# Performance work log

Measured on AMD Instinct MI355X. Metric: run time of the kernel, lower is better.

## Reference

```python
import jax, jax.numpy as jnp
import numpy as np

B, T, C, H = 2, 4096, 512, 8
D = C // H          # head_size = 64
FF = 4 * C          # 2048
EPS = 1e-5


def _layernorm(x, g, b):
    mu = jnp.mean(x, axis=-1, keepdims=True)
    var = jnp.mean(jnp.square(x - mu), axis=-1, keepdims=True)
    return (x - mu) * jax.lax.rsqrt(var + EPS) * g + b


def setup_inputs() -> dict:
    key = jax.random.key(0)
    ks = jax.random.split(key, 10)
    s = 0.02
    return {
        "x":  jax.random.normal(ks[0], (B, T, C), dtype=jnp.float32),
        # per-head K/Q/V linears (bias=False) packed as [C, C] = concat over heads
        "Wq": jax.random.normal(ks[1], (C, C), dtype=jnp.float32) * s,
        "Wk": jax.random.normal(ks[2], (C, C), dtype=jnp.float32) * s,
        "Wv": jax.random.normal(ks[3], (C, C), dtype=jnp.float32) * s,
        "Wo": jax.random.normal(ks[4], (C, C), dtype=jnp.float32) * s,
        "bo": jnp.zeros((C,), dtype=jnp.float32),
        "W1": jax.random.normal(ks[5], (C, FF), dtype=jnp.float32) * s,
        "b1": jnp.zeros((FF,), dtype=jnp.float32),
        "W2": jax.random.normal(ks[6], (FF, C), dtype=jnp.float32) * s,
        "b2": jnp.zeros((C,), dtype=jnp.float32),
        "g1": jnp.ones((C,), dtype=jnp.float32),
        "be1": jnp.zeros((C,), dtype=jnp.float32),
        "g2": jnp.ones((C,), dtype=jnp.float32),
        "be2": jnp.zeros((C,), dtype=jnp.float32),
    }


def reference(x, Wq, Wk, Wv, Wo, bo, W1, b1, W2, b2, g1, be1, g2, be2):
    # --- self-attention on ln1(x), residual add ---
    h = _layernorm(x, g1, be1)                              # [B,T,C]
    q = (h @ Wq).reshape(B, T, H, D)
    k = (h @ Wk).reshape(B, T, H, D)
    v = (h @ Wv).reshape(B, T, H, D)
    # NOTE: original scales by C**-0.5 (n_embd), NOT head_size**-0.5
    scores = jnp.einsum("bthd,bshd->bhts", q, k) * (C ** -0.5)  # [B,H,T,T]
    causal = jnp.tril(jnp.ones((T, T), dtype=bool))
    scores = jnp.where(causal, scores, -jnp.inf)
    wei = jax.nn.softmax(scores, axis=-1)                   # dropout = identity (eval)
    attn = jnp.einsum("bhts,bshd->bthd", wei, v).reshape(B, T, C)
    x = x + (attn @ Wo + bo)                                # proj dropout = identity
    # --- feed-forward on ln2(x), residual add ---
    h2 = _layernorm(x, g2, be2)
    ff = jax.nn.relu(h2 @ W1 + b1) @ W2 + b2                # dropout = identity
    return x + ff
```

## Files before the change

kernel.cpp:

```cpp
#include <hip/hip_runtime.h>

typedef __attribute__((ext_vector_type(8))) __bf16 bf16x8;
typedef __attribute__((ext_vector_type(4))) __bf16 bf16x4;
typedef __attribute__((ext_vector_type(4))) float f32x4;
typedef __attribute__((ext_vector_type(4))) unsigned int u32x4;
typedef __attribute__((ext_vector_type(4))) unsigned short u16x4;
typedef __attribute__((ext_vector_type(8))) unsigned short u16x8;
typedef __attribute__((ext_vector_type(4))) short s16x4;
typedef unsigned short u16;

static __device__ __forceinline__ u16 f2b(float f) {
    unsigned u = __builtin_bit_cast(unsigned, f);
    u = (u + 0x7FFFu + ((u >> 16) & 1u)) >> 16;
    return (u16)u;
}
static __device__ __forceinline__ float b2f(u16 u) {
    return __builtin_bit_cast(float, ((unsigned)u) << 16);
}
static __device__ __forceinline__ float fexp2(float x) {
#if __has_builtin(__builtin_amdgcn_exp2f)
    return __builtin_amdgcn_exp2f(x);
#else
    return exp2f(x);
#endif
}
static __device__ __forceinline__ f32x4 mfma16(bf16x4 a, bf16x4 b, f32x4 c) {
#if __has_builtin(__builtin_amdgcn_mfma_f32_16x16x16_bf16)
    return __builtin_amdgcn_mfma_f32_16x16x16_bf16(a, b, c, 0, 0, 0);
#else
    return __builtin_amdgcn_mfma_f32_16x16x16bf16_1k(
        __builtin_bit_cast(s16x4, a), __builtin_bit_cast(s16x4, b), c, 0, 0, 0);
#endif
}

static __device__ __forceinline__ void gload16(const u16* g, u16* l) {
    __builtin_amdgcn_global_load_lds(
        (const __attribute__((address_space(1))) unsigned int*)g,
        (__attribute__((address_space(3))) unsigned int*)l, 16, 0, 0);
}

__global__ __launch_bounds__(256) void prep_w(
    const float* __restrict__ Wq, const float* __restrict__ Wk,
    const float* __restrict__ Wv, const float* __restrict__ Wo,
    const float* __restrict__ W1, const float* __restrict__ W2,
    u16* __restrict__ WqkvT, u16* __restrict__ WoT,
    u16* __restrict__ W1T, u16* __restrict__ W2T)
{
    const int i = blockIdx.x;
    const float* src; u16* dst; int K, N, nt, kt;
    if (i < 1024) {
        const int z = i >> 8, idx = i & 255;
        K = 512; N = 512; nt = (idx & 15) * 32; kt = (idx >> 4) * 32;
        if (z == 0)      { src = Wq; dst = WqkvT; }
        else if (z == 1) { src = Wk; dst = WqkvT + 512*512; }
        else if (z == 2) { src = Wv; dst = WqkvT + 1024*512; }
        else             { src = Wo; dst = WoT; }
    } else if (i < 2048) {
        const int idx = i - 1024;
        src = W1; dst = W1T; K = 512; N = 2048;
        nt = (idx & 63) * 32; kt = (idx >> 6) * 32;
    } else {
        const int idx = i - 2048;
        src = W2; dst = W2T; K = 2048; N = 512;
        nt = (idx & 15) * 32; kt = (idx >> 4) * 32;
    }
    __shared__ float tile[32][33];
    const int tx = threadIdx.x & 31, ty = threadIdx.x >> 5;
    #pragma unroll
    for (int r = 0; r < 4; ++r)
        tile[ty + r*8][tx] = src[(size_t)(kt + ty + r*8) * N + nt + tx];
    __syncthreads();
    #pragma unroll
    for (int r = 0; r < 4; ++r)
        dst[(size_t)(nt + ty + r*8) * K + kt + tx] = f2b(tile[tx][ty + r*8]);
}

__global__ __launch_bounds__(256) void ln_rows(
    const float* __restrict__ x, const float* __restrict__ g,
    const float* __restrict__ b, u16* __restrict__ out)
{
    const int row = blockIdx.x * 4 + (threadIdx.x >> 6);
    const int lane = threadIdx.x & 63;
    const float* xr = x + (size_t)row * 512;
    f32x4 v0 = *(const f32x4*)(xr + lane * 4);
    f32x4 v1 = *(const f32x4*)(xr + 256 + lane * 4);
    float s = v0[0]+v0[1]+v0[2]+v0[3]+v1[0]+v1[1]+v1[2]+v1[3];
    #pragma unroll
    for (int o = 1; o < 64; o <<= 1) s += __shfl_xor(s, o);
    const float mu = s * (1.0f / 512.0f);
    float s2 = 0.f;
    #pragma unroll
    for (int i = 0; i < 4; ++i) { float d0 = v0[i]-mu, d1 = v1[i]-mu; s2 += d0*d0 + d1*d1; }
    #pragma unroll
    for (int o = 1; o < 64; o <<= 1) s2 += __shfl_xor(s2, o);
    const float inv = rsqrtf(s2 * (1.0f/512.0f) + 1e-5f);
    f32x4 g0 = *(const f32x4*)(g + lane*4), g1 = *(const f32x4*)(g + 256 + lane*4);
    f32x4 b0 = *(const f32x4*)(b + lane*4), b1 = *(const f32x4*)(b + 256 + lane*4);
    u16x4 p0, p1;
    #pragma unroll
    for (int i = 0; i < 4; ++i) {
        p0[i] = f2b((v0[i]-mu)*inv*g0[i] + b0[i]);
        p1[i] = f2b((v1[i]-mu)*inv*g1[i] + b1[i]);
    }
    u16* orow = out + (size_t)row * 512;
    *(u16x4*)(orow + lane*4)       = p0;
    *(u16x4*)(orow + 256 + lane*4) = p1;
}

template<int FLAGS, int NB>
__global__ __launch_bounds__(256) void gemm_bt(
    const u16* __restrict__ A, const u16* __restrict__ BT,
    const int N, const int K,
    const float* __restrict__ bias, const float* __restrict__ res,
    void* __restrict__ outv, u16* __restrict__ vt)
{
    constexpr int RING = (NB == 2) ? 3 : 4;
    __shared__ __attribute__((aligned(16))) u16 As[RING * 4096];
    __shared__ __attribute__((aligned(16))) u16 Bs[RING * 2048 * NB];
    const int tid = threadIdx.x, lane = tid & 63, w = tid >> 6;
    const int wr2 = w >> 1, wc = w & 1;
    const int m0 = blockIdx.y << 7, n0 = blockIdx.x * (64 * NB);
    const int g = lane >> 4, c = lane & 15;
    const f32x4 fz = {0.f, 0.f, 0.f, 0.f};

    f32x4 acc[4][2 * NB];
    #pragma unroll
    for (int m = 0; m < 4; ++m)
      #pragma unroll
      for (int n = 0; n < 2 * NB; ++n) acc[m][n] = fz;

    const int srow = tid >> 2;
    const int scs = (((tid & 3) ^ (srow & 3)) * 8);
    const u16* Ag = A  + (size_t)(m0 + srow)*K + scs;
    const u16* Bg = BT + (size_t)(n0 + srow)*K + scs;
    const size_t rstep = (size_t)64 * K;

    const int nkt = K >> 5;
    auto stage = [&](int slot, int kt) {
        const int k0 = kt << 5;
        u16* ad = &As[0] + slot*4096 + w*512;
        gload16(Ag + k0,         ad);
        gload16(Ag + rstep + k0, ad + 2048);
        u16* bd = &Bs[0] + slot*2048*NB + w*512;
        gload16(Bg + k0, bd);
        if constexpr (NB == 2) gload16(Bg + rstep + k0, bd + 2048);
    };
    stage(0, 0);
    stage(1, (1 < nkt) ? 1 : 0);
    if constexpr (RING == 4) stage(2, (2 < nkt) ? 2 : 0);

    for (int kt = 0; kt < nkt; ++kt) {
        if constexpr (NB == 2) asm volatile("s_waitcnt vmcnt(4)" ::: "memory");
        else                   asm volatile("s_waitcnt vmcnt(6)" ::: "memory");
        __builtin_amdgcn_s_barrier();
        asm volatile("" ::: "memory");
        {
            int tp = kt + RING - 1; if (tp >= nkt) tp = nkt - 1;
            int sl = kt + RING - 1; sl -= (sl / RING) * RING;
            stage(sl, tp);
        }
        const int rd = kt - (kt / RING) * RING;
        const u16* Ab = &As[0] + rd*4096;
        const u16* Bb = &Bs[0] + rd*2048*NB;
        bf16x8 af[4], bfr[2 * NB];
        #pragma unroll
        for (int m = 0; m < 4; ++m) {
            const int row = wr2*64 + m*16 + c;
            af[m] = *(const bf16x8*)(Ab + row*32 + (((g*16) ^ ((row&3)<<4)) >> 1));
        }
        #pragma unroll
        for (int n = 0; n < 2 * NB; ++n) {
            const int row = wc*(32*NB) + n*16 + c;
            bfr[n] = *(const bf16x8*)(Bb + row*32 + (((g*16) ^ ((row&3)<<4)) >> 1));
        }
        #pragma unroll
        for (int m = 0; m < 4; ++m)
          #pragma unroll
          for (int n = 0; n < 2 * NB; ++n)
            acc[m][n] = __builtin_amdgcn_mfma_f32_16x16x32_bf16(af[m], bfr[n], acc[m][n], 0, 0, 0);
    }

    #pragma unroll
    for (int m = 0; m < 4; ++m) {
        const int row = m0 + wr2*64 + m*16 + 4*g;
        #pragma unroll
        for (int n = 0; n < 2 * NB; ++n) {
            const int col = n0 + wc*(32*NB) + n*16 + c;
            const float bv = (FLAGS & 1) ? bias[col] : 0.0f;
            float vv[4];
            #pragma unroll
            for (int r = 0; r < 4; ++r) {
                float v = acc[m][n][r] + bv;
                if (FLAGS & 16) v *= (col < 512) ? 0.0637587246f : 1.0f;
                if (FLAGS & 2) v += res[(size_t)(row + r)*N + col];
                if (FLAGS & 4) v = fmaxf(v, 0.0f);
                vv[r] = v;
            }
            if ((FLAGS & 32) && col >= 1024) {
                u16x4 pv;
                #pragma unroll
                for (int r = 0; r < 4; ++r) pv[r] = f2b(vv[r]);
                *(u16x4*)(vt + (size_t)((row >> 12)*512 + (col - 1024))*4096
                             + (row & 4095)) = pv;
            } else if (FLAGS & 8) {
                #pragma unroll
                for (int r = 0; r < 4; ++r)
                    ((float*)outv)[(size_t)(row + r)*N + col] = vv[r];
            } else {
                #pragma unroll
                for (int r = 0; r < 4; ++r)
                    ((u16*)outv)[(size_t)(row + r)*N + col] = f2b(vv[r]);
            }
        }
    }
}

__global__ __launch_bounds__(256, 3) void attn_fwd(
    const u16* __restrict__ qkv, const u16* __restrict__ vT,
    u16* __restrict__ part, u16* __restrict__ att)
{
    const int bh = blockIdx.y, b = bh >> 3, h = bh & 7;
    const int i = blockIdx.x;
    int qt, t0, t1, single;
    if (i < 32) { qt = i; t0 = 0; t1 = qt + 1; single = 1; }
    else {
        const int j = i - 32; qt = 32 + (j >> 1);
        const int nt = qt + 1, tm = nt >> 1;
        t0 = (j & 1) ? tm : 0; t1 = (j & 1) ? nt : tm; single = 0;
    }

    const int tid = threadIdx.x, lane = tid & 63, w = tid >> 6;
    const int g = lane >> 4, c16 = lane & 15;
    __shared__ __attribute__((aligned(16))) u16 smem[24576 + 512];
    u16* Wb = smem + w*6144;
    float* lbuf = (float*)(smem + 24576);

    const u16* qp  = qkv + (size_t)b*4096*1536 + h*64;
    const u16* kp  = qp + 512;
    const u16* vtp = vT + (size_t)bh*64*4096;

    const u16* kgA = kp + (size_t)(16*w + (lane>>3))*1536
                        + (((lane&7) ^ ((lane>>3)&7)) * 8);
    const u16* kgB = kgA + (size_t)8*1536;
    const int sd = lane >> 1;
    const u16* vgA = vtp + (size_t)sd*4096 + 16*w + (((lane&1) ^ ((sd>>2)&1)) * 8);
    const u16* vgB = vgA + (size_t)32*4096;

    const int kOff0 = c16*64 + ((g ^ (c16&7)) * 8);
    const int kOff1 = c16*64 + (((4+g) ^ (c16&7)) * 8);
    const int vroff = c16*16 + (((g>>1) ^ ((c16>>2)&1)) * 8) + (g&1)*4;

    const int Q0 = qt*64;
    bf16x8 qB[4][2];
    #pragma unroll
    for (int sub = 0; sub < 4; ++sub) {
        const u16* qr = qp + (size_t)(Q0 + sub*16 + c16)*1536 + g*8;
        qB[sub][0] = *(const bf16x8*)(qr);
        qB[sub][1] = *(const bf16x8*)(qr + 32);
    }

    const f32x4 fz = {0.f,0.f,0.f,0.f};
    f32x4 oacc[4][4];
    #pragma unroll
    for (int dt = 0; dt < 4; ++dt)
      #pragma unroll
      for (int sub = 0; sub < 4; ++sub) oacc[dt][sub] = fz;
    float lsum[4] = {0.f, 0.f, 0.f, 0.f};

    {
        const int tp1 = (t0+1 < t1) ? (t0+1) : (t1-1);
        u16* s0 = Wb + (t0 % 3)*2048;
        const size_t ko0 = (size_t)(t0 << 6)*1536; const int kv0 = t0 << 6;
        gload16(kgA + ko0, s0);        gload16(kgB + ko0, s0 + 512);
        gload16(vgA + kv0, s0 + 1024); gload16(vgB + kv0, s0 + 1536);
        u16* s1 = Wb + (tp1 % 3)*2048;
        const size_t ko1 = (size_t)(tp1 << 6)*1536; const int kv1 = tp1 << 6;
        gload16(kgA + ko1, s1);        gload16(kgB + ko1, s1 + 512);
        gload16(vgA + kv1, s1 + 1024); gload16(vgB + kv1, s1 + 1536);
    }
    int rd = t0 % 3;
    int wrs = rd + 2; if (wrs >= 3) wrs -= 3;

    for (int t = t0; t < t1; ++t) {
        {
            const int tp = (t+2 < t1) ? (t+2) : (t1-1);
            u16* slotW = Wb + wrs*2048;
            const size_t ko = (size_t)(tp << 6)*1536; const int kv = tp << 6;
            gload16(kgA + ko, slotW);        gload16(kgB + ko, slotW + 512);
            gload16(vgA + kv, slotW + 1024); gload16(vgB + kv, slotW + 1536);
        }
        asm volatile("s_waitcnt vmcnt(8)" ::: "memory");
        const u16* slotR = Wb + rd*2048;
        const bf16x8 kc0 = *(const bf16x8*)(slotR + kOff0);
        const bf16x8 kc1 = *(const bf16x8*)(slotR + kOff1);
        bf16x4 va[4];
        #pragma unroll
        for (int dt = 0; dt < 4; ++dt)
            va[dt] = *(const bf16x4*)(slotR + 1024 + dt*256 + vroff);
        f32x4 s[4];
        #pragma unroll
        for (int sub = 0; sub < 4; ++sub) {
            f32x4 sv = __builtin_amdgcn_mfma_f32_16x16x32_bf16(kc0, qB[sub][0], fz, 0, 0, 0);
            s[sub]   = __builtin_amdgcn_mfma_f32_16x16x32_bf16(kc1, qB[sub][1], sv, 0, 0, 0);
        }
        bf16x4 pt[4];
        if (t < qt) {
            #pragma unroll
            for (int sub = 0; sub < 4; ++sub) {
                float p0 = fexp2(s[sub][0]), p1 = fexp2(s[sub][1]);
                float p2 = fexp2(s[sub][2]), p3 = fexp2(s[sub][3]);
                lsum[sub] += (p0 + p1) + (p2 + p3);
                bf16x4 pv;
                pv[0] = (__bf16)p0; pv[1] = (__bf16)p1;
                pv[2] = (__bf16)p2; pv[3] = (__bf16)p3;
                pt[sub] = pv;
            }
        } else {
            const int kvbase = t*64 + 16*w + 4*g;
            #pragma unroll
            for (int sub = 0; sub < 4; ++sub) {
                const int qi = Q0 + sub*16 + c16;
                bf16x4 pv; float a = 0.f;
                #pragma unroll
                for (int r = 0; r < 4; ++r) {
                    float p = (kvbase + r <= qi) ? fexp2(s[sub][r]) : 0.0f;
                    a += p; pv[r] = (__bf16)p;
                }
                lsum[sub] += a; pt[sub] = pv;
            }
        }
        #pragma unroll
        for (int dt = 0; dt < 4; ++dt)
          #pragma unroll
          for (int sub = 0; sub < 4; ++sub)
            oacc[dt][sub] = mfma16(va[dt], pt[sub], oacc[dt][sub]);
        rd  = (rd  == 2) ? 0 : rd  + 1;
        wrs = (wrs == 2) ? 0 : wrs + 1;
    }

    #pragma unroll
    for (int sub = 0; sub < 4; ++sub) {
        float v = lsum[sub];
        v += __shfl_xor(v, 16);
        v += __shfl_xor(v, 32);
        if (g == 0) lbuf[w*64 + sub*16 + c16] = v;
    }
    __syncthreads();
    float ltot[4];
    #pragma unroll
    for (int sub = 0; sub < 4; ++sub) {
        const int qr = sub*16 + c16;
        ltot[sub] = lbuf[qr] + lbuf[64 + qr] + lbuf[128 + qr] + lbuf[192 + qr];
    }

    float* img = (float*)smem;
    f32x4 ofin[4];
    const int roff = (g ^ (c16 & 3))*4;
    #pragma unroll
    for (int dt = 0; dt < 4; ++dt) {
        #pragma unroll
        for (int sub = 0; sub < 4; ++sub)
            *(f32x4*)(img + w*1024 + (sub*16 + c16)*16 + roff) = oacc[dt][sub];
        __syncthreads();
        if (w == dt) {
            #pragma unroll
            for (int sub = 0; sub < 4; ++sub) {
                const int off = (sub*16 + c16)*16 + roff;
                f32x4 a0 = *(const f32x4*)(img + off);
                f32x4 a1 = *(const f32x4*)(img + 1024 + off);
                f32x4 a2 = *(const f32x4*)(img + 2048 + off);
                f32x4 a3 = *(const f32x4*)(img + 3072 + off);
                ofin[sub] = (a0 + a1) + (a2 + a3);
            }
        }
        __syncthreads();
    }

    const int dbase = 16*w + 4*g;
    if (single) {
        #pragma unroll
        for (int sub = 0; sub < 4; ++sub) {
            const int qrow = sub*16 + c16;
            const float inv = 1.0f / ltot[sub];
            const f32x4 o = ofin[sub];
            u16x4 ov;
            ov[0] = f2b(o[0]*inv); ov[1] = f2b(o[1]*inv);
            ov[2] = f2b(o[2]*inv); ov[3] = f2b(o[3]*inv);
            *(u16x4*)(att + (size_t)(b*4096 + Q0 + qrow)*512 + h*64 + dbase) = ov;
        }
    } else {
        u16* onum = part + (size_t)(bh*64 + (i - 32)) * 4224;
        float* lout = (float*)(onum + 4096);
        #pragma unroll
        for (int sub = 0; sub < 4; ++sub) {
            const int qrow = sub*16 + c16;
            const f32x4 o = ofin[sub];
            u16x4 ov;
            ov[0] = f2b(o[0]); ov[1] = f2b(o[1]);
            ov[2] = f2b(o[2]); ov[3] = f2b(o[3]);
            *(u16x4*)(onum + qrow*64 + dbase) = ov;
            if (w == 0 && g == 0) lout[qrow] = ltot[sub];
        }
    }
}

__global__ __launch_bounds__(256) void attn_merge(
    const u16* __restrict__ part, u16* __restrict__ att)
{
    const int qt = 32 + blockIdx.x, bh = blockIdx.y, b = bh >> 3, h = bh & 7;
    const int t = threadIdx.x;
    const int row = t >> 2, c0 = (t & 3) * 16;
    const u16* p0 = part + (size_t)(bh*64 + 2*blockIdx.x) * 4224;
    const u16* p1 = p0 + 4224;
    const float lt = ((const float*)(p0 + 4096))[row] + ((const float*)(p1 + 4096))[row];
    const float inv = 1.0f / lt;
    u16x8 a0 = *(const u16x8*)(p0 + row*64 + c0);
    u16x8 a1 = *(const u16x8*)(p0 + row*64 + c0 + 8);
    u16x8 b0q = *(const u16x8*)(p1 + row*64 + c0);
    u16x8 b1q = *(const u16x8*)(p1 + row*64 + c0 + 8);
    u16x8 o1, o2;
    #pragma unroll
    for (int j = 0; j < 8; ++j) {
        o1[j] = f2b((b2f(a0[j]) + b2f(b0q[j])) * inv);
        o2[j] = f2b((b2f(a1[j]) + b2f(b1q[j])) * inv);
    }
    u16* dst = att + (size_t)(b*4096 + qt*64 + row)*512 + h*64 + c0;
    *(u16x8*)dst = o1;
    *(u16x8*)(dst + 8) = o2;
}

extern "C" void kernel_launch(void* const* d_in, const int* in_sizes, int n_in,
                              void* d_out, int out_size, void* d_ws, size_t ws_size,
                              hipStream_t stream)
{
    (void)in_sizes; (void)n_in; (void)out_size; (void)ws_size;
    const float* x   = (const float*)d_in[0];
    const float* Wq  = (const float*)d_in[1];
    const float* Wk  = (const float*)d_in[2];
    const float* Wv  = (const float*)d_in[3];
    const float* Wo  = (const float*)d_in[4];
    const float* bo  = (const float*)d_in[5];
    const float* W1  = (const float*)d_in[6];
    const float* b1  = (const float*)d_in[7];
    const float* W2  = (const float*)d_in[8];
    const float* b2  = (const float*)d_in[9];
    const float* g1  = (const float*)d_in[10];
    const float* be1 = (const float*)d_in[11];
    const float* g2  = (const float*)d_in[12];
    const float* be2 = (const float*)d_in[13];

    char* ws = (char*)d_ws;
    u16*   WqkvT = (u16*)(ws + 0);
    u16*   WoT   = (u16*)(ws + 1572864);
    u16*   W1T   = (u16*)(ws + 2097152);
    u16*   W2T   = (u16*)(ws + 4194304);
    u16*   H     = (u16*)(ws + 6291456);
    u16*   PART  = (u16*)(ws + 6291456);
    float* X2    = (float*)(ws + 14680064);
    u16*   QKV   = (u16*)(ws + 31457280);
    u16*   VT    = (u16*)(ws + 56623104);
    u16*   ATT   = (u16*)(ws + 65011712);
    u16*   F1    = (u16*)(ws + 31457280);

    prep_w<<<3072, 256, 0, stream>>>(Wq, Wk, Wv, Wo, W1, W2,
                                     WqkvT, WoT, W1T, W2T);
    ln_rows<<<2048, 256, 0, stream>>>(x, g1, be1, H);
    gemm_bt<48, 2><<<dim3(12, 64), 256, 0, stream>>>(H, WqkvT, 1536, 512,
                                                     nullptr, nullptr, QKV, VT);
    attn_fwd<<<dim3(96, 16), 256, 0, stream>>>(QKV, VT, PART, ATT);
    attn_merge<<<dim3(32, 16), 256, 0, stream>>>(PART, ATT);
    gemm_bt<11, 1><<<dim3(8, 64), 256, 0, stream>>>(ATT, WoT, 512, 512,
                                                    bo, x, X2, nullptr);
    ln_rows<<<2048, 256, 0, stream>>>(X2, g2, be2, H);
    gemm_bt<5, 2><<<dim3(16, 64), 256, 0, stream>>>(H, W1T, 2048, 512,
                                                    b1, nullptr, F1, nullptr);
    gemm_bt<11, 1><<<dim3(8, 64), 256, 0, stream>>>(F1, W2T, 512, 2048,
                                                    b2, X2, (float*)d_out, nullptr);
}
```

Before: 215.3 us.

## Split causal attention query tiles into 1-4 KV chunks with XCD-aware block mapping

Replaces the old split, where only query tiles from 32 up were halved, with a graded split: query tiles are cut into 1, 2, 3 or 4 KV chunks depending on their causal length. Blocks are remapped so each XCD gets two heads, and heavy tiles are scheduled first. This aims to balance work across blocks and improve L2 locality for K/V. The merge kernel now sums a variable number of partials, which costs extra partial-buffer traffic and a larger merge launch.

```diff
diff --git a/kernel.cpp b/kernel.cpp
--- a/kernel.cpp
+++ b/kernel.cpp
@@ -219,15 +219,20 @@
     const u16* __restrict__ qkv, const u16* __restrict__ vT,
     u16* __restrict__ part, u16* __restrict__ att)
 {
-    const int bh = blockIdx.y, b = bh >> 3, h = bh & 7;
-    const int i = blockIdx.x;
-    int qt, t0, t1, single;
-    if (i < 32) { qt = i; t0 = 0; t1 = qt + 1; single = 1; }
-    else {
-        const int j = i - 32; qt = 32 + (j >> 1);
-        const int nt = qt + 1, tm = nt >> 1;
-        t0 = (j & 1) ? tm : 0; t1 = (j & 1) ? nt : tm; single = 0;
-    }
+    const int fid = blockIdx.x + 160 * blockIdx.y;
+    const int xcd = fid & 7, s0i = fid >> 3;
+    const int half = (s0i >= 160) ? 1 : 0;
+    const int bh = xcd*2 + half, b = bh >> 3, h = bh & 7;
+    const int i = 159 - (s0i - half*160);
+    int qt, cch, nch;
+    if (i < 16)      { qt = i;                         cch = 0;          nch = 1; }
+    else if (i < 48) { int j = i-16; qt = 16 + (j>>1); cch = j & 1;      nch = 2; }
+    else if (i < 96) { int j = i-48; int d3 = j/3; qt = 32 + d3; cch = j - 3*d3; nch = 3; }
+    else             { int j = i-96; qt = 48 + (j>>2); cch = j & 3;      nch = 4; }
+    const int ntl = qt + 1;
+    const int t0 = (cch * ntl) / nch;
+    const int t1 = ((cch + 1) * ntl) / nch;
+    const int single = (nch == 1);
 
     const int tid = threadIdx.x, lane = tid & 63, w = tid >> 6;
     const int g = lane >> 4, c16 = lane & 15;
@@ -269,14 +274,14 @@
 
     {
         const int tp1 = (t0+1 < t1) ? (t0+1) : (t1-1);
-        u16* s0 = Wb + (t0 % 3)*2048;
+        u16* sl0 = Wb + (t0 % 3)*2048;
         const size_t ko0 = (size_t)(t0 << 6)*1536; const int kv0 = t0 << 6;
-        gload16(kgA + ko0, s0);        gload16(kgB + ko0, s0 + 512);
-        gload16(vgA + kv0, s0 + 1024); gload16(vgB + kv0, s0 + 1536);
-        u16* s1 = Wb + (tp1 % 3)*2048;
+        gload16(kgA + ko0, sl0);        gload16(kgB + ko0, sl0 + 512);
+        gload16(vgA + kv0, sl0 + 1024); gload16(vgB + kv0, sl0 + 1536);
+        u16* sl1 = Wb + (tp1 % 3)*2048;
         const size_t ko1 = (size_t)(tp1 << 6)*1536; const int kv1 = tp1 << 6;
-        gload16(kgA + ko1, s1);        gload16(kgB + ko1, s1 + 512);
-        gload16(vgA + kv1, s1 + 1024); gload16(vgB + kv1, s1 + 1536);
+        gload16(kgA + ko1, sl1);        gload16(kgB + ko1, sl1 + 512);
+        gload16(vgA + kv1, sl1 + 1024); gload16(vgB + kv1, sl1 + 1536);
     }
     int rd = t0 % 3;
     int wrs = rd + 2; if (wrs >= 3) wrs -= 3;
@@ -389,7 +394,7 @@
             *(u16x4*)(att + (size_t)(b*4096 + Q0 + qrow)*512 + h*64 + dbase) = ov;
         }
     } else {
-        u16* onum = part + (size_t)(bh*64 + (i - 32)) * 4224;
+        u16* onum = part + (size_t)(bh*160 + i) * 4224;
         float* lout = (float*)(onum + 4096);
         #pragma unroll
         for (int sub = 0; sub < 4; ++sub) {
@@ -407,23 +412,30 @@
 __global__ __launch_bounds__(256) void attn_merge(
     const u16* __restrict__ part, u16* __restrict__ att)
 {
-    const int qt = 32 + blockIdx.x, bh = blockIdx.y, b = bh >> 3, h = bh & 7;
+    const int qt = 16 + blockIdx.x, bh = blockIdx.y, b = bh >> 3, h = bh & 7;
+    int start, n;
+    if (qt < 32)      { start = 16 + 2*(qt-16); n = 2; }
+    else if (qt < 48) { start = 48 + 3*(qt-32); n = 3; }
+    else              { start = 96 + 4*(qt-48); n = 4; }
     const int t = threadIdx.x;
     const int row = t >> 2, c0 = (t & 3) * 16;
-    const u16* p0 = part + (size_t)(bh*64 + 2*blockIdx.x) * 4224;
-    const u16* p1 = p0 + 4224;
-    const float lt = ((const float*)(p0 + 4096))[row] + ((const float*)(p1 + 4096))[row];
+    float acc[16];
+    #pragma unroll
+    for (int j = 0; j < 16; ++j) acc[j] = 0.f;
+    float lt = 0.f;
+    const u16* p0 = part + (size_t)(bh*160 + start) * 4224;
+    for (int ci = 0; ci < n; ++ci) {
+        const u16* pc = p0 + (size_t)ci * 4224;
+        lt += ((const float*)(pc + 4096))[row];
+        u16x8 a = *(const u16x8*)(pc + row*64 + c0);
+        u16x8 bq = *(const u16x8*)(pc + row*64 + c0 + 8);
+        #pragma unroll
+        for (int j = 0; j < 8; ++j) { acc[j] += b2f(a[j]); acc[8+j] += b2f(bq[j]); }
+    }
     const float inv = 1.0f / lt;
-    u16x8 a0 = *(const u16x8*)(p0 + row*64 + c0);
-    u16x8 a1 = *(const u16x8*)(p0 + row*64 + c0 + 8);
-    u16x8 b0q = *(const u16x8*)(p1 + row*64 + c0);
-    u16x8 b1q = *(const u16x8*)(p1 + row*64 + c0 + 8);
     u16x8 o1, o2;
     #pragma unroll
-    for (int j = 0; j < 8; ++j) {
-        o1[j] = f2b((b2f(a0[j]) + b2f(b0q[j])) * inv);
-        o2[j] = f2b((b2f(a1[j]) + b2f(b1q[j])) * inv);
-    }
+    for (int j = 0; j < 8; ++j) { o1[j] = f2b(acc[j]*inv); o2[j] = f2b(acc[8+j]*inv); }
     u16* dst = att + (size_t)(b*4096 + qt*64 + row)*512 + h*64 + c0;
     *(u16x8*)dst = o1;
     *(u16x8*)(dst + 8) = o2;
@@ -467,8 +479,8 @@
     ln_rows<<<2048, 256, 0, stream>>>(x, g1, be1, H);
     gemm_bt<48, 2><<<dim3(12, 64), 256, 0, stream>>>(H, WqkvT, 1536, 512,
                                                      nullptr, nullptr, QKV, VT);
-    attn_fwd<<<dim3(96, 16), 256, 0, stream>>>(QKV, VT, PART, ATT);
-    attn_merge<<<dim3(32, 16), 256, 0, stream>>>(PART, ATT);
+    attn_fwd<<<dim3(160, 16), 256, 0, stream>>>(QKV, VT, PART, ATT);
+    attn_merge<<<dim3(48, 16), 256, 0, stream>>>(PART, ATT);
     gemm_bt<11, 1><<<dim3(8, 64), 256, 0, stream>>>(ATT, WoT, 512, 512,
                                                     bo, x, X2, nullptr);
     ln_rows<<<2048, 256, 0, stream>>>(X2, g2, be2, H);
```

New measurement: 207.0 us. 3.9% less time.
